# Performance work log

Measured on AMD Instinct MI355X. Metric: run time of the kernel, lower is better.

The kernel has to match this reference:

```python
import jax, jax.numpy as jnp
import numpy as np
import math

B, L, CS, CZ = 1, 512, 256, 128
H, CH, PQ, PV = 8, 32, 4, 8
NUM_BLOCKS = 8
CAT = H * CH + H * PV * 3 + H * PV + H * CZ  # 1536


def _ln(x, g, b, eps=1e-5):
    mu = jnp.mean(x, -1, keepdims=True)
    var = jnp.mean((x - mu) ** 2, -1, keepdims=True)
    return (x - mu) * jax.lax.rsqrt(var + eps) * g + b


def _quat_to_rot(bq, cq, dq):
    # BackboneUpdate: quaternion with implicit a=1, normalized (AF2 Alg. 23)
    norm = jnp.sqrt(1.0 + bq * bq + cq * cq + dq * dq)
    a = 1.0 / norm
    b = bq / norm
    c = cq / norm
    d = dq / norm
    return jnp.stack([
        jnp.stack([a * a + b * b - c * c - d * d, 2 * (b * c - a * d), 2 * (b * d + a * c)], -1),
        jnp.stack([2 * (b * c + a * d), a * a - b * b + c * c - d * d, 2 * (c * d - a * b)], -1),
        jnp.stack([2 * (b * d - a * c), 2 * (c * d + a * b), a * a - b * b - c * c + d * d], -1),
    ], -2)


def _forward(s, z, mask, ln_s_g, ln_s_b, ln_z_g, ln_z_b, w_init, b_init,
             ln_ipa_g, ln_ipa_b, ln_tr_g, ln_tr_b,
             wq, bq, wk, bk, wv, bv, wqp, bqp, wkp, bkp, wvp, bvp,
             wpb, head_w, wo, bo, wt1, bt1, wt2, bt2, wt3, bt3, wbb, bbb):
    s0 = _ln(s, ln_s_g, ln_s_b)
    zn = _ln(z, ln_z_g, ln_z_b)
    sc = s0 @ w_init + b_init
    R = jnp.broadcast_to(jnp.eye(3, dtype=s.dtype), (B, L, 3, 3))
    t = jnp.zeros((B, L, 3), s.dtype)
    wL = math.sqrt(1.0 / 3.0)
    wC = math.sqrt(2.0 / (9.0 * PQ))
    gamma = jax.nn.softplus(head_w)  # [H]
    pair_bias = jnp.einsum('bijc,ch->bhij', zn, wpb)
    mask_bias = (mask[:, None, None, :] - 1.0) * 1e9
    for i in range(NUM_BLOCKS):
        # ---- Invariant Point Attention (AF2 Alg. 22, shared weights) ----
        q = (sc @ wq + bq).reshape(B, L, H, CH)
        k = (sc @ wk + bk).reshape(B, L, H, CH)
        v = (sc @ wv + bv).reshape(B, L, H, CH)
        qp = (sc @ wqp + bqp).reshape(B, L, H, PQ, 3)
        kp = (sc @ wkp + bkp).reshape(B, L, H, PQ, 3)
        vp = (sc @ wvp + bvp).reshape(B, L, H, PV, 3)
        tb = t[:, :, None, None, :]
        qpg = jnp.einsum('blij,blhpj->blhpi', R, qp) + tb  # local -> global
        kpg = jnp.einsum('blij,blhpj->blhpi', R, kp) + tb
        vpg = jnp.einsum('blij,blhpj->blhpi', R, vp) + tb
        scal = jnp.einsum('bihc,bjhc->bhij', q, k) / math.sqrt(CH)
        # sum_p ||qpg_i - kpg_j||^2 via |q|^2 + |k|^2 - 2 q.k (avoids [B,L,L,H,P,3])
        qk = jnp.einsum('bihpx,bjhpx->bhij', qpg, kpg)
        qn = jnp.moveaxis(jnp.sum(qpg ** 2, axis=(-2, -1)), -1, 1)  # [B,H,L]
        kn = jnp.moveaxis(jnp.sum(kpg ** 2, axis=(-2, -1)), -1, 1)
        d2 = qn[..., :, None] + kn[..., None, :] - 2.0 * qk  # [B,H,L,L]
        logits = wL * (scal + pair_bias - 0.5 * wC * gamma[None, :, None, None] * d2) + mask_bias
        a = jax.nn.softmax(logits, axis=-1)
        o = jnp.einsum('bhij,bjhc->bihc', a, v).reshape(B, L, H * CH)
        optg = jnp.einsum('bhij,bjhpx->bihpx', a, vpg)
        optl = jnp.einsum('blji,blhpj->blhpi', R, optg - tb)  # R^T (o - t)
        onrm = jnp.sqrt(jnp.sum(optl ** 2, -1) + 1e-8)  # [B,L,H,PV]
        opair = jnp.einsum('bhij,bijc->bihc', a, zn).reshape(B, L, H * CZ)
        cat = jnp.concatenate([o, optl.reshape(B, L, H * PV * 3), onrm.reshape(B, L, H * PV), opair], -1)
        ipa_up = cat @ wo + bo
        sc = _ln(sc + ipa_up, ln_ipa_g, ln_ipa_b)  # dropout = identity (eval)
        # ---- transition ----
        tr = jax.nn.relu(sc @ wt1 + bt1)
        tr = jax.nn.relu(tr @ wt2 + bt2)
        tr = (tr @ wt3 + bt3) * mask[..., None]
        sc = _ln(sc + tr, ln_tr_g, ln_tr_b)
        # ---- backbone update + frame composition ----
        upd = sc @ wbb + bbb  # [B,L,6]
        dR = _quat_to_rot(upd[..., 0], upd[..., 1], upd[..., 2])
        dt = upd[..., 3:6] * mask[..., None]
        t = jnp.einsum('blij,blj->bli', R, dt) + t
        R = jnp.einsum('blij,bljk->blik', R, dR)
        if i < NUM_BLOCKS - 1:
            R = jax.lax.stop_gradient(R)  # stop_rotation_gradients
    return sc, R, t


def setup_inputs() -> dict:
    key = jax.random.key(0)
    ks = jax.random.split(key, 20)
    w = lambda k, shape, sc=0.05: jax.random.normal(k, shape, jnp.float32) * sc
    inp = dict(
        s=jax.random.normal(ks[0], (B, L, CS), jnp.float32),
        z=jax.random.normal(ks[1], (B, L, L, CZ), jnp.float32),
        mask=jnp.ones((B, L), jnp.float32),
        ln_s_g=jnp.ones((CS,), jnp.float32), ln_s_b=jnp.zeros((CS,), jnp.float32),
        ln_z_g=jnp.ones((CZ,), jnp.float32), ln_z_b=jnp.zeros((CZ,), jnp.float32),
        w_init=w(ks[2], (CS, CS)), b_init=jnp.zeros((CS,), jnp.float32),
        ln_ipa_g=jnp.ones((CS,), jnp.float32), ln_ipa_b=jnp.zeros((CS,), jnp.float32),
        ln_tr_g=jnp.ones((CS,), jnp.float32), ln_tr_b=jnp.zeros((CS,), jnp.float32),
        wq=w(ks[3], (CS, H * CH)), bq=jnp.zeros((H * CH,), jnp.float32),
        wk=w(ks[4], (CS, H * CH)), bk=jnp.zeros((H * CH,), jnp.float32),
        wv=w(ks[5], (CS, H * CH)), bv=jnp.zeros((H * CH,), jnp.float32),
        wqp=w(ks[6], (CS, H * PQ * 3)), bqp=jnp.zeros((H * PQ * 3,), jnp.float32),
        wkp=w(ks[7], (CS, H * PQ * 3)), bkp=jnp.zeros((H * PQ * 3,), jnp.float32),
        wvp=w(ks[8], (CS, H * PV * 3)), bvp=jnp.zeros((H * PV * 3,), jnp.float32),
        wpb=w(ks[9], (CZ, H)),
        head_w=jnp.zeros((H,), jnp.float32),
        wo=w(ks[10], (CAT, CS), 0.02), bo=jnp.zeros((CS,), jnp.float32),
        wt1=w(ks[11], (CS, CS)), bt1=jnp.zeros((CS,), jnp.float32),
        wt2=w(ks[12], (CS, CS)), bt2=jnp.zeros((CS,), jnp.float32),
        wt3=w(ks[13], (CS, CS)), bt3=jnp.zeros((CS,), jnp.float32),
        wbb=w(ks[14], (CS, 6)), bbb=jnp.zeros((6,), jnp.float32),
    )
    return inp


def reference(s, z, mask, ln_s_g, ln_s_b, ln_z_g, ln_z_b, w_init, b_init,
              ln_ipa_g, ln_ipa_b, ln_tr_g, ln_tr_b,
              wq, bq, wk, bk, wv, bv, wqp, bqp, wkp, bkp, wvp, bvp,
              wpb, head_w, wo, bo, wt1, bt1, wt2, bt2, wt3, bt3, wbb, bbb):
    return _forward(s, z, mask, ln_s_g, ln_s_b, ln_z_g, ln_z_b, w_init, b_init,
                    ln_ipa_g, ln_ipa_b, ln_tr_g, ln_tr_b,
                    wq, bq, wk, bk, wv, bv, wqp, bqp, wkp, bkp, wvp, bvp,
                    wpb, head_w, wo, bo, wt1, bt1, wt2, bt2, wt3, bt3, wbb, bbb)
```

## Files before the change

### kernel.cpp

```cpp
#include <hip/hip_runtime.h>
#include <hip/hip_bf16.h>
#include <hip/hip_fp16.h>
#include <math.h>

#define Lq 512
#define CSd 256
#define CZd 128
#define Hd 8
#define CHd 32
#define PQd 4
#define PVd 8
#define CATd 1536
#define NPROJ 1152

typedef __attribute__((ext_vector_type(4))) float floatx4;
typedef __attribute__((ext_vector_type(8))) short shortx8;

#define OFF_SC      0
#define OFF_PB      393216
#define OFF_P       1441792
#define OFF_QN      2031616
#define OFF_KN      2035712
#define OFF_A16     2039808
#define OFF_CAT     4136960
#define OFF_S0      4923392
#define OFF_R       5054464
#define OFF_T       5059072
#define OFF_GAMMA   5060608
#define OFF_MASKB   5060616
#define OFF_BCAT    5061128
#define OFF_WINITP  5062280
#define OFF_WT1P    5127816
#define OFF_WT2P    5193352
#define OFF_WT3P    5258888
#define OFF_WOP     5324424
#define OFF_WCATP   5717640
#define OFF_QP      6012552
#define OFF_KP      6274696
#define OFF_VP      6536840
#define OFF_SCA16   6798984
#define OFF_ZNT     6930056

#define CAT_LO 786432

#define WLC 0.57735026918962576f
#define WCC 0.23570226039551584f
#define ISC 0.17677669529663687f

__device__ __forceinline__ float wave_sum(float v){
  #pragma unroll
  for (int m=32; m; m>>=1) v += __shfl_xor(v, m);
  return v;
}
__device__ __forceinline__ short f2bf(float v){
  __hip_bfloat16 h = (__hip_bfloat16)v;
  return __builtin_bit_cast(short, h);
}
__device__ __forceinline__ float bf2f(short s){
  unsigned u = ((unsigned)(unsigned short)s) << 16;
  return __builtin_bit_cast(float, u);
}
__device__ __forceinline__ __hip_bfloat16 s2b(short s){
  return __builtin_bit_cast(__hip_bfloat16, s);
}
__device__ __forceinline__ void cat_store(short* __restrict__ catA16, int k, int row, float v){
  size_t off = (((size_t)(k>>5)*512 + row)*4 + ((k>>3)&3))*8 + (k&7);
  short hh = f2bf(v);
  catA16[off]          = hh;
  catA16[off + CAT_LO] = f2bf(v - bf2f(hh));
}

__global__ __launch_bounds__(256) void k_setup(
    const float* __restrict__ bq, const float* __restrict__ bk, const float* __restrict__ bv,
    const float* __restrict__ bqp, const float* __restrict__ bkp, const float* __restrict__ bvp,
    const float* __restrict__ head_w, const float* __restrict__ mask,
    float* __restrict__ bcat, float* __restrict__ gamma,
    float* __restrict__ maskb, float* __restrict__ R, float* __restrict__ t){
  int k = blockIdx.x*256 + threadIdx.x;
  if (k < NPROJ){
    float v;
    if      (k < 256) v = bq[k];
    else if (k < 512) v = bk[k-256];
    else if (k < 768) v = bv[k-512];
    else if (k < 864) v = bqp[k-768];
    else if (k < 960) v = bkp[k-864];
    else              v = bvp[k-960];
    bcat[k] = v;
    return;
  }
  k -= NPROJ;
  if (k < Hd){ gamma[k] = log1pf(expf(head_w[k])); return; }
  k -= Hd;
  if (k < Lq){ maskb[k] = (mask[k] - 1.f)*1e9f; return; }
  k -= Lq;
  if (k < Lq){
    #pragma unroll
    for (int ii=0; ii<9; ii++) R[k*9+ii] = (ii==0||ii==4||ii==8) ? 1.f : 0.f;
    t[k*3] = 0.f; t[k*3+1] = 0.f; t[k*3+2] = 0.f;
  }
}

__global__ __launch_bounds__(256) void k_pack(
    const float* __restrict__ W, int K, int N, __hip_bfloat16* __restrict__ out){
  int idx = blockIdx.x*256 + threadIdx.x;
  if (idx >= K*N) return;
  int j = idx & 7, lane = (idx>>3) & 63, rest = idx >> 9;
  int nt = N >> 4;
  int tn = rest % nt, tk = rest / nt;
  int k = tk*32 + (lane>>4)*8 + j;
  int n = tn*16 + (lane&15);
  float v = W[(size_t)k*N + n];
  short h = f2bf(v);
  short l = f2bf(v - bf2f(h));
  size_t base = (size_t)rest*1024 + (idx & 511);
  out[base]       = s2b(h);
  out[base + 512] = s2b(l);
}

__global__ __launch_bounds__(256) void k_pack_cat(
    const float* __restrict__ wq, const float* __restrict__ wk, const float* __restrict__ wv,
    const float* __restrict__ wqp, const float* __restrict__ wkp, const float* __restrict__ wvp,
    __hip_bfloat16* __restrict__ out){
  int idx = blockIdx.x*256 + threadIdx.x;
  if (idx >= CSd*NPROJ) return;
  int j = idx & 7, lane = (idx>>3) & 63, rest = idx >> 9;
  const int nt = NPROJ >> 4;
  int tn = rest % nt, tk = rest / nt;
  int k = tk*32 + (lane>>4)*8 + j;
  int n = tn*16 + (lane&15);
  float v;
  if      (n < 256) v = wq[k*256 + n];
  else if (n < 512) v = wk[k*256 + n-256];
  else if (n < 768) v = wv[k*256 + n-512];
  else if (n < 864) v = wqp[k*96 + n-768];
  else if (n < 960) v = wkp[k*96 + n-864];
  else              v = wvp[k*192 + n-960];
  short h = f2bf(v);
  short l = f2bf(v - bf2f(h));
  size_t base = (size_t)rest*1024 + (idx & 511);
  out[base]       = s2b(h);
  out[base + 512] = s2b(l);
}

template<int NST>
__global__ __launch_bounds__(256) void k_gemm_mfma(
    const float* __restrict__ A, int K,
    const __hip_bfloat16* __restrict__ Bp, int N,
    const float* __restrict__ bias,
    float* __restrict__ Cf,
    int relu, const float* __restrict__ rowscale){
  int tid = threadIdx.x;
  int wave = tid>>6, lane = tid&63;
  int i0 = blockIdx.y*64 + wave*16;
  int n0 = blockIdx.x*(NST*16);
  int quad = lane>>4, l16 = lane&15;
  floatx4 acc[NST] = {};
  const int ntiles = N >> 4;
  const float* arow = A + (size_t)(i0 + l16)*K + quad*8;
  const __hip_bfloat16* bbase = Bp + ((size_t)(n0>>4))*1024 + (size_t)(lane&63)*8;
  for (int k0=0; k0<K; k0+=32){
    float4 v0 = *(const float4*)(arow + k0);
    float4 v1 = *(const float4*)(arow + k0 + 4);
    float av[8] = {v0.x,v0.y,v0.z,v0.w,v1.x,v1.y,v1.z,v1.w};
    shortx8 ahi, alo;
    #pragma unroll
    for (int j=0; j<8; j++){
      short h = f2bf(av[j]);
      ahi[j] = h;
      alo[j] = f2bf(av[j] - bf2f(h));
    }
    const __hip_bfloat16* bt = bbase + (size_t)(k0>>5)*ntiles*1024;
    #pragma unroll
    for (int s=0; s<NST; s++){
      shortx8 bhi = *(const shortx8*)(bt + s*1024);
      shortx8 blo = *(const shortx8*)(bt + s*1024 + 512);
      acc[s] = __builtin_amdgcn_mfma_f32_16x16x32_bf16(ahi, bhi, acc[s], 0, 0, 0);
      acc[s] = __builtin_amdgcn_mfma_f32_16x16x32_bf16(alo, bhi, acc[s], 0, 0, 0);
      acc[s] = __builtin_amdgcn_mfma_f32_16x16x32_bf16(ahi, blo, acc[s], 0, 0, 0);
    }
  }
  #pragma unroll
  for (int s=0; s<NST; s++){
    int n = n0 + s*16 + l16;
    float bs = bias ? bias[n] : 0.f;
    #pragma unroll
    for (int r=0; r<4; r++){
      int m = i0 + quad*4 + r;
      float v = acc[s][r] + bs;
      if (relu) v = fmaxf(v, 0.f);
      if (rowscale) v *= rowscale[m];
      Cf[(size_t)m*N + n] = v;
    }
  }
}

__global__ __launch_bounds__(256) void k_cvtA(
    const float* __restrict__ sc, short* __restrict__ scA16){
  int idx = blockIdx.x*256 + threadIdx.x;
  int i = idx>>5, c5 = idx&31;
  int c0 = c5*8, kc = c5>>2, quad = c5&3;
  float4 v0 = *(const float4*)(sc + (size_t)i*CSd + c0);
  float4 v1 = *(const float4*)(sc + (size_t)i*CSd + c0 + 4);
  float av[8] = {v0.x,v0.y,v0.z,v0.w,v1.x,v1.y,v1.z,v1.w};
  shortx8 hi, lo;
  #pragma unroll
  for (int j=0; j<8; j++){
    short h = f2bf(av[j]);
    hi[j] = h; lo[j] = f2bf(av[j] - bf2f(h));
  }
  size_t off = ((size_t)(kc*512 + i)*4 + quad)*8;
  *(shortx8*)(scA16 + off)          = hi;
  *(shortx8*)(scA16 + off + 131072) = lo;
}

__global__ __launch_bounds__(256) void k_gemm_proj(
    const short* __restrict__ scA16,
    const __hip_bfloat16* __restrict__ Bp,
    const float* __restrict__ bias,
    float* __restrict__ Cf){
  int tid = threadIdx.x;
  int wave = tid>>6, lane = tid&63;
  int i0 = blockIdx.y*64 + wave*16;
  int n0 = blockIdx.x*32;
  int quad = lane>>4, l16 = lane&15;
  floatx4 acc[2] = {};
  const short* abase = scA16 + ((size_t)(i0 + l16)*4 + quad)*8;
  const __hip_bfloat16* bbase = Bp + ((size_t)(n0>>4))*1024 + (size_t)lane*8;
  #pragma unroll
  for (int kc=0; kc<8; kc++){
    shortx8 ahi = *(const shortx8*)(abase + kc*16384);
    shortx8 alo = *(const shortx8*)(abase + kc*16384 + 131072);
    const __hip_bfloat16* bt = bbase + (size_t)kc*72*1024;
    #pragma unroll
    for (int s=0; s<2; s++){
      shortx8 bhi = *(const shortx8*)(bt + s*1024);
      shortx8 blo = *(const shortx8*)(bt + s*1024 + 512);
      acc[s] = __builtin_amdgcn_mfma_f32_16x16x32_bf16(ahi, bhi, acc[s], 0, 0, 0);
      acc[s] = __builtin_amdgcn_mfma_f32_16x16x32_bf16(alo, bhi, acc[s], 0, 0, 0);
      acc[s] = __builtin_amdgcn_mfma_f32_16x16x32_bf16(ahi, blo, acc[s], 0, 0, 0);
    }
  }
  #pragma unroll
  for (int s=0; s<2; s++){
    int n = n0 + s*16 + l16;
    float bs = bias[n];
    #pragma unroll
    for (int r=0; r<4; r++)
      Cf[(size_t)(i0 + quad*4 + r)*NPROJ + n] = acc[s][r] + bs;
  }
}

__global__ __launch_bounds__(256) void k_gemm_ipa(
    const short* __restrict__ catA16, const __hip_bfloat16* __restrict__ Bp,
    const float* __restrict__ bias, float* __restrict__ C0, float* __restrict__ C1){
  int tid = threadIdx.x;
  int wave = tid>>6, lane = tid&63;
  int ks = blockIdx.y >> 3;
  int i0 = (blockIdx.y & 7)*64 + wave*16;
  int n0 = blockIdx.x*16;
  int quad = lane>>4, l16 = lane&15;
  floatx4 acc = {};
  const short* abase = catA16 + (size_t)(ks*24)*16384 + (size_t)(i0 + l16)*32 + quad*8;
  const __hip_bfloat16* bbase = Bp + ((size_t)(ks*24*16 + (n0>>4)))*1024 + (size_t)lane*8;
  #pragma unroll
  for (int kc=0; kc<24; kc++){
    shortx8 ahi = *(const shortx8*)(abase + kc*16384);
    shortx8 alo = *(const shortx8*)(abase + kc*16384 + CAT_LO);
    const __hip_bfloat16* bt = bbase + (size_t)kc*16*1024;
    shortx8 bhi = *(const shortx8*)bt;
    shortx8 blo = *(const shortx8*)(bt + 512);
    acc = __builtin_amdgcn_mfma_f32_16x16x32_bf16(ahi, bhi, acc, 0, 0, 0);
    acc = __builtin_amdgcn_mfma_f32_16x16x32_bf16(alo, bhi, acc, 0, 0, 0);
    acc = __builtin_amdgcn_mfma_f32_16x16x32_bf16(ahi, blo, acc, 0, 0, 0);
  }
  float* C = ks ? C1 : C0;
  int n = n0 + l16;
  float bs = ks ? 0.f : bias[n];
  #pragma unroll
  for (int r=0; r<4; r++)
    C[(size_t)(i0 + quad*4 + r)*CSd + n] = acc[r] + bs;
}

__global__ __launch_bounds__(256) void k_addln(
    const float* __restrict__ x, const float* __restrict__ y,
    const float* __restrict__ g, const float* __restrict__ b,
    float* __restrict__ out){
  __shared__ float red[4];
  int row = blockIdx.x, tid = threadIdx.x;
  float v = x[row*CSd + tid];
  if (y) v += y[row*CSd + tid];
  int wid = tid>>6, lane = tid&63;
  float s = wave_sum(v);
  if (lane==0) red[wid] = s;
  __syncthreads();
  float mu = (red[0]+red[1]+red[2]+red[3]) * (1.f/CSd);
  __syncthreads();
  float d = v - mu;
  float s2 = wave_sum(d*d);
  if (lane==0) red[wid] = s2;
  __syncthreads();
  float var = (red[0]+red[1]+red[2]+red[3]) * (1.f/CSd);
  float rs = rsqrtf(var + 1e-5f);
  out[row*CSd + tid] = d*rs*g[tid] + b[tid];
}

__global__ __launch_bounds__(1024, 4) void k_lnz_pb(
    const float* __restrict__ z, const float* __restrict__ g, const float* __restrict__ b,
    const float* __restrict__ wpb, __half* __restrict__ pb, __hip_bfloat16* __restrict__ znt){
  __shared__ float Zt[64*129];
  __shared__ float wpbht[8*129];
  __shared__ float gl[128], bl[128];
  int tid = threadIdx.x;
  size_t row0 = (size_t)blockIdx.x*64;
  int ib = (int)(row0 >> 9), j0 = (int)(row0 & 511);
  {
    int c = tid>>3, h = tid&7;
    wpbht[h*129 + c] = wpb[tid];
  }
  if (tid < 128){ gl[tid] = g[tid]; bl[tid] = b[tid]; }
  {
    int w = tid>>6, lane = tid&63;
    #pragma unroll
    for (int it=0; it<4; it++){
      int row = it*16 + w;
      const float2 v = *(const float2*)(z + (row0+row)*(size_t)CZd + lane*2);
      Zt[row*129 + lane*2]     = v.x;
      Zt[row*129 + lane*2 + 1] = v.y;
    }
  }
  __syncthreads();
  {
    int r = tid>>4, q = tid&15;
    int rot = 2*(q>>2);
    float S1=0.f, S2=0.f;
    float zv[8];
    #pragma unroll
    for (int i=0; i<8; i++){
      int ii = (i + rot) & 7;
      float v = Zt[r*129 + q*8 + ii];
      zv[i] = v;
      S1 += v; S2 += v*v;
    }
    S1 += __shfl_xor(S1,1); S2 += __shfl_xor(S2,1);
    S1 += __shfl_xor(S1,2); S2 += __shfl_xor(S2,2);
    S1 += __shfl_xor(S1,4); S2 += __shfl_xor(S2,4);
    S1 += __shfl_xor(S1,8); S2 += __shfl_xor(S2,8);
    float mu = S1 * (1.f/128.f);
    float var = S2 * (1.f/128.f) - mu*mu;
    float rs = rsqrtf(var + 1e-5f);
    float d[8] = {};
    #pragma unroll
    for (int i=0; i<8; i++){
      int ii = (i + rot) & 7;
      int c = q*8 + ii;
      float znv = (zv[i]-mu)*rs*gl[c] + bl[c];
      Zt[r*129 + c] = znv;
      #pragma unroll
      for (int h=0; h<8; h++) d[h] += znv * wpbht[h*129 + c];
    }
    #pragma unroll
    for (int h=0; h<8; h++){
      d[h] += __shfl_xor(d[h],1);
      d[h] += __shfl_xor(d[h],2);
      d[h] += __shfl_xor(d[h],4);
      d[h] += __shfl_xor(d[h],8);
    }
    if (q == 0){
      #pragma unroll
      for (int h=0; h<8; h++)
        pb[((size_t)(h*Lq + ib))*Lq + j0 + r] = __float2half(d[h]);
    }
  }
  __syncthreads();
  {
    int c = tid>>3, jg = tid&7;
    int jb = jg*8;
    unsigned int o[4];
    #pragma unroll
    for (int k=0; k<4; k++){
      float z0 = Zt[(jb+2*k)*129 + c];
      float z1 = Zt[(jb+2*k+1)*129 + c];
      o[k] = ((unsigned int)(unsigned short)f2bf(z0)) |
             (((unsigned int)(unsigned short)f2bf(z1)) << 16);
    }
    unsigned short* zo = (unsigned short*)znt;
    uint4 pk = make_uint4(o[0],o[1],o[2],o[3]);
    *(uint4*)(zo + ((size_t)(ib*128 + c))*512 + j0 + jb) = pk;
  }
}

__global__ __launch_bounds__(256) void k_packqkv(
    const float* __restrict__ P, const float* __restrict__ R, const float* __restrict__ t,
    const float* __restrict__ gamma, int zfill,
    float* __restrict__ Qp, __hip_bfloat16* __restrict__ Kp, __hip_bfloat16* __restrict__ Vp,
    float* __restrict__ qn, float* __restrict__ kn){
  int idx = blockIdx.x*256 + threadIdx.x;
  int region = idx >> 15;
  int rem = idx & 32767;
  if (region == 0){
    int oct = rem & 7, h = (rem>>3)&7, j = rem>>6;
    float v[8] = {0.f,0.f,0.f,0.f,0.f,0.f,0.f,0.f};
    const float* Prow = P + (size_t)j*NPROJ;
    if (oct < 4){
      float4 a = *(const float4*)(Prow + 256 + h*CHd + oct*8);
      float4 b4 = *(const float4*)(Prow + 256 + h*CHd + oct*8 + 4);
      v[0]=a.x; v[1]=a.y; v[2]=a.z; v[3]=a.w; v[4]=b4.x; v[5]=b4.y; v[6]=b4.z; v[7]=b4.w;
    } else if (oct < 6){
      const float* kp = Prow + 864 + h*12;
      float4 k0 = *(const float4*)kp;
      float4 k1 = *(const float4*)(kp+4);
      float4 k2 = *(const float4*)(kp+8);
      float kv[12] = {k0.x,k0.y,k0.z,k0.w,k1.x,k1.y,k1.z,k1.w,k2.x,k2.y,k2.z,k2.w};
      float Rl[9];
      #pragma unroll
      for (int ii=0; ii<9; ii++) Rl[ii] = R[j*9+ii];
      float tv[3] = {t[j*3], t[j*3+1], t[j*3+2]};
      float gvals[12];
      #pragma unroll
      for (int p=0; p<4; p++)
        #pragma unroll
        for (int ax=0; ax<3; ax++)
          gvals[p*3+ax] = Rl[ax*3]*kv[p*3] + Rl[ax*3+1]*kv[p*3+1] + Rl[ax*3+2]*kv[p*3+2] + tv[ax];
      if (oct == 4){
        #pragma unroll
        for (int m=0; m<8; m++) v[m] = gvals[m];
      } else {
        #pragma unroll
        for (int m=0; m<4; m++) v[m] = gvals[8+m];
        float acc = 0.f;
        #pragma unroll
        for (int m=0; m<12; m++) acc += gvals[m]*gvals[m];
        kn[j*Hd + h] = acc;
      }
    } else {
      if (!zfill) return;
    }
    shortx8 hi, lo;
    #pragma unroll
    for (int m=0; m<8; m++){
      short hh = f2bf(v[m]);
      hi[m] = hh; lo[m] = f2bf(v[m] - bf2f(hh));
    }
    int kc = oct>>2, jt = j>>4, l16 = j&15, quad = oct&3;
    size_t base = (size_t)((h*2+kc)*32 + jt)*1024 + (quad*16+l16)*8;
    short* kp16 = (short*)Kp;
    *(shortx8*)(kp16 + base)       = hi;
    *(shortx8*)(kp16 + base + 512) = lo;
  } else if (region == 1){
    int n = rem & 63, h = (rem>>6)&7, jg = rem>>9;
    int jb = jg*8;
    float v[8] = {0.f,0.f,0.f,0.f,0.f,0.f,0.f,0.f};
    if (n < 32){
      #pragma unroll
      for (int m=0; m<8; m++) v[m] = P[(size_t)(jb+m)*NPROJ + 512 + h*CHd + n];
    } else if (n < 56){
      int p = (n-32)/3, ax = (n-32)%3;
      #pragma unroll
      for (int m=0; m<8; m++){
        int j = jb+m;
        const float* vp = P + (size_t)j*NPROJ + 960 + h*24 + p*3;
        const float* Rr = R + j*9 + ax*3;
        v[m] = Rr[0]*vp[0] + Rr[1]*vp[1] + Rr[2]*vp[2] + t[j*3+ax];
      }
    } else {
      if (!zfill) return;
    }
    shortx8 hi, lo;
    #pragma unroll
    for (int m=0; m<8; m++){
      short hh = f2bf(v[m]);
      hi[m] = hh; lo[m] = f2bf(v[m] - bf2f(hh));
    }
    int kc2 = jg>>2, w = n>>4, l16 = n&15, quad = jg&3;
    size_t base = (size_t)((h*16+kc2)*4 + w)*1024 + (quad*16+l16)*8;
    short* vp16 = (short*)Vp;
    *(shortx8*)(vp16 + base)       = hi;
    *(shortx8*)(vp16 + base + 512) = lo;
  } else {
    int oct = rem & 7, h = (rem>>3)&7, i = rem>>6;
    float v[8] = {0.f,0.f,0.f,0.f,0.f,0.f,0.f,0.f};
    const float* Prow = P + (size_t)i*NPROJ;
    if (oct < 4){
      float4 a = *(const float4*)(Prow + h*CHd + oct*8);
      float4 b4 = *(const float4*)(Prow + h*CHd + oct*8 + 4);
      const float sc = WLC*ISC;
      v[0]=a.x*sc; v[1]=a.y*sc; v[2]=a.z*sc; v[3]=a.w*sc;
      v[4]=b4.x*sc; v[5]=b4.y*sc; v[6]=b4.z*sc; v[7]=b4.w*sc;
    } else if (oct < 6){
      const float* qp = Prow + 768 + h*12;
      float4 k0 = *(const float4*)qp;
      float4 k1 = *(const float4*)(qp+4);
      float4 k2 = *(const float4*)(qp+8);
      float kv[12] = {k0.x,k0.y,k0.z,k0.w,k1.x,k1.y,k1.z,k1.w,k2.x,k2.y,k2.z,k2.w};
      float Rl[9];
      #pragma unroll
      for (int ii=0; ii<9; ii++) Rl[ii] = R[i*9+ii];
      float tv[3] = {t[i*3], t[i*3+1], t[i*3+2]};
      float gvals[12];
      #pragma unroll
      for (int p=0; p<4; p++)
        #pragma unroll
        for (int ax=0; ax<3; ax++)
          gvals[p*3+ax] = Rl[ax*3]*kv[p*3] + Rl[ax*3+1]*kv[p*3+1] + Rl[ax*3+2]*kv[p*3+2] + tv[ax];
      float sc = WLC*WCC*gamma[h];
      if (oct == 4){
        #pragma unroll
        for (int m=0; m<8; m++) v[m] = gvals[m]*sc;
      } else {
        #pragma unroll
        for (int m=0; m<4; m++) v[m] = gvals[8+m]*sc;
        float acc = 0.f;
        #pragma unroll
        for (int m=0; m<12; m++) acc += gvals[m]*gvals[m];
        qn[i*Hd + h] = acc;
      }
    } else {
      if (!zfill) return;
    }
    float* qrow = Qp + ((size_t)h*512 + i)*64 + oct*8;
    *(float4*)qrow       = make_float4(v[0],v[1],v[2],v[3]);
    *(float4*)(qrow + 4) = make_float4(v[4],v[5],v[6],v[7]);
  }
}

__global__ __launch_bounds__(1024) void k_attn(
    const float* __restrict__ Qp, const __hip_bfloat16* __restrict__ Kp,
    const __hip_bfloat16* __restrict__ Vp,
    const float* __restrict__ qn, const float* __restrict__ kn,
    const __half* __restrict__ pb, const float* __restrict__ maskb,
    const float* __restrict__ gamma,
    const float* __restrict__ R, const float* __restrict__ t,
    __hip_bfloat16* __restrict__ a16hi,
    short* __restrict__ catA16){
  __shared__ float At[16][516];
  __shared__ short AbfH[16*4*16*8];
  __shared__ short AbfL[16*4*16*8];
  __shared__ float Pv[3][16][68];
  __shared__ float Ot[16][36];
  __shared__ float qnL[16];
  int tid = threadIdx.x;
  int i0 = blockIdx.x*16, h = blockIdx.y;
  int wave = tid>>6, lane = tid&63, quad = lane>>4, l16 = lane&15;
  int kg = wave>>2, ng = wave&3;
  float gam = gamma[h];
  float coef = 0.5f*WLC*WCC*gam;
  if (tid < 16) qnL[tid] = qn[(i0+tid)*Hd + h];
  __syncthreads();
  const float* qrow = Qp + ((size_t)h*512 + i0 + l16)*64 + quad*8;
  shortx8 qhi[2], qlo[2];
  #pragma unroll
  for (int kc=0; kc<2; kc++){
    float4 v0 = *(const float4*)(qrow + kc*32);
    float4 v1 = *(const float4*)(qrow + kc*32 + 4);
    float av[8] = {v0.x,v0.y,v0.z,v0.w,v1.x,v1.y,v1.z,v1.w};
    #pragma unroll
    for (int j=0; j<8; j++){
      short hh = f2bf(av[j]);
      qhi[kc][j] = hh; qlo[kc][j] = f2bf(av[j] - bf2f(hh));
    }
  }
  #pragma unroll
  for (int it=0; it<2; it++){
    int jt = it*16 + wave;
    floatx4 acc = {};
    #pragma unroll
    for (int kc=0; kc<2; kc++){
      const __hip_bfloat16* bt = Kp + (size_t)((h*2+kc)*32 + jt)*1024 + lane*8;
      shortx8 bhi = *(const shortx8*)bt;
      shortx8 blo = *(const shortx8*)(bt + 512);
      acc = __builtin_amdgcn_mfma_f32_16x16x32_bf16(qhi[kc], bhi, acc, 0, 0, 0);
      acc = __builtin_amdgcn_mfma_f32_16x16x32_bf16(qlo[kc], bhi, acc, 0, 0, 0);
      acc = __builtin_amdgcn_mfma_f32_16x16x32_bf16(qhi[kc], blo, acc, 0, 0, 0);
    }
    int j = jt*16 + l16;
    float knj = kn[j*Hd + h];
    float mbj = maskb[j];
    #pragma unroll
    for (int r=0; r<4; r++){
      int i = quad*4 + r;
      float pbv = __half2float(pb[((size_t)(h*Lq) + i0 + i)*Lq + j]);
      At[i][j] = acc[r] + WLC*pbv + mbj - coef*(qnL[i] + knj);
    }
  }
  __syncthreads();
  {
    int w = wave;
    float v[8];
    float m = -1e30f;
    #pragma unroll
    for (int k=0; k<8; k++){ v[k] = At[w][lane + 64*k]; m = fmaxf(m, v[k]); }
    #pragma unroll
    for (int msk=32; msk; msk>>=1) m = fmaxf(m, __shfl_xor(m, msk));
    float ssum = 0.f;
    #pragma unroll
    for (int k=0; k<8; k++){ float e = __expf(v[k]-m); v[k]=e; ssum += e; }
    #pragma unroll
    for (int msk=32; msk; msk>>=1) ssum += __shfl_xor(ssum, msk);
    float inv = 1.f/ssum;
    #pragma unroll
    for (int k=0; k<8; k++){
      int cc = lane + 64*k;
      float p = v[k]*inv;
      short hh = f2bf(p);
      short ll = f2bf(p - bf2f(hh));
      a16hi[(((size_t)(i0+w)*16 + (cc>>5))*8 + h)*32 + (cc&31)] = s2b(hh);
      int off = ((((cc>>5)*4 + ((cc>>3)&3))*16 + w)<<3) + (cc&7);
      AbfH[off] = hh;
      AbfL[off] = ll;
    }
  }
  __syncthreads();
  floatx4 acc2 = {};
  #pragma unroll
  for (int kk=0; kk<4; kk++){
    int kc2 = kg*4 + kk;
    int aoff = (((kc2*4 + quad)*16 + l16))<<3;
    shortx8 ahi = *(const shortx8*)&AbfH[aoff];
    shortx8 alo = *(const shortx8*)&AbfL[aoff];
    const __hip_bfloat16* bt = Vp + (size_t)((h*16+kc2)*4 + ng)*1024 + lane*8;
    shortx8 bhi = *(const shortx8*)bt;
    shortx8 blo = *(const shortx8*)(bt + 512);
    acc2 = __builtin_amdgcn_mfma_f32_16x16x32_bf16(ahi, bhi, acc2, 0, 0, 0);
    acc2 = __builtin_amdgcn_mfma_f32_16x16x32_bf16(alo, bhi, acc2, 0, 0, 0);
    acc2 = __builtin_amdgcn_mfma_f32_16x16x32_bf16(ahi, blo, acc2, 0, 0, 0);
  }
  if (kg > 0){
    #pragma unroll
    for (int r=0;r<4;r++) Pv[kg-1][quad*4+r][ng*16+l16] = acc2[r];
  }
  __syncthreads();
  if (kg == 0){
    int n = ng*16 + l16;
    #pragma unroll
    for (int r=0;r<4;r++){
      int i = quad*4+r;
      float v = acc2[r] + Pv[0][i][n] + Pv[1][i][n] + Pv[2][i][n];
      if (n < 32) cat_store(catA16, h*CHd + n, i0+i, v);
      else        Ot[i][n-32] = v;
    }
  }
  __syncthreads();
  if (tid < 128){
    int i = tid>>3, p = tid&7, gi = i0+i;
    float o0 = Ot[i][p*3], o1 = Ot[i][p*3+1], o2 = Ot[i][p*3+2];
    float d0 = o0 - t[gi*3], d1 = o1 - t[gi*3+1], d2 = o2 - t[gi*3+2];
    const float* Rm = R + gi*9;
    float l0 = Rm[0]*d0 + Rm[3]*d1 + Rm[6]*d2;
    float l1 = Rm[1]*d0 + Rm[4]*d1 + Rm[7]*d2;
    float l2 = Rm[2]*d0 + Rm[5]*d1 + Rm[8]*d2;
    int kb = 256 + h*24 + p*3;
    cat_store(catA16, kb,   gi, l0);
    cat_store(catA16, kb+1, gi, l1);
    cat_store(catA16, kb+2, gi, l2);
    cat_store(catA16, 448 + h*8 + p, gi, sqrtf(l0*l0 + l1*l1 + l2*l2 + 1e-8f));
  }
}

__global__ __launch_bounds__(512) void k_opair_mfma(
    const __hip_bfloat16* __restrict__ a16hi,
    const __hip_bfloat16* __restrict__ znt, short* __restrict__ catA16){
  int i = blockIdx.x;
  int tid = threadIdx.x;
  int wave = tid>>6, lane = tid&63, quad = lane>>4, l16 = lane&15;
  int nt = wave;
  floatx4 acc = {};
  const __hip_bfloat16* abase_h = a16hi + ((size_t)i*16*8 + (l16&7))*32 + quad*8;
  const __hip_bfloat16* zb = znt + ((size_t)i*128 + nt*16 + l16)*512 + quad*8;
  #pragma unroll
  for (int kt=0; kt<16; kt++){
    shortx8 ah = *(const shortx8*)(abase_h + kt*256);
    shortx8 b0 = *(const shortx8*)(zb + kt*32);
    acc = __builtin_amdgcn_mfma_f32_16x16x32_bf16(ah, b0, acc, 0, 0, 0);
  }
  if (quad < 2){
    #pragma unroll
    for (int r=0; r<4; r++){
      int h = quad*4 + r;
      cat_store(catA16, 512 + h*CZd + nt*16 + l16, i, acc[r]);
    }
  }
}

__device__ __forceinline__ void gemm_bf16w(
    const short* __restrict__ AHp, const short* __restrict__ ALp,
    short* __restrict__ OH, short* __restrict__ OL, float (*Yf)[260],
    const __hip_bfloat16* __restrict__ Wp, const float* __restrict__ bias,
    bool relu, int tid){
  int wave = tid>>6, lane = tid&63, quad = lane>>4, l16 = lane&15;
  floatx4 acc = {};
  #pragma unroll
  for (int kc=0; kc<8; kc++){
    int aoff = (((kc*4 + quad)*16 + l16))<<3;
    shortx8 ahi = *(const shortx8*)&AHp[aoff];
    shortx8 alo = *(const shortx8*)&ALp[aoff];
    const __hip_bfloat16* bt = Wp + (size_t)(kc*16 + wave)*1024 + lane*8;
    shortx8 bhi = *(const shortx8*)bt;
    shortx8 blo = *(const shortx8*)(bt + 512);
    acc = __builtin_amdgcn_mfma_f32_16x16x32_bf16(ahi, bhi, acc, 0, 0, 0);
    acc = __builtin_amdgcn_mfma_f32_16x16x32_bf16(alo, bhi, acc, 0, 0, 0);
    acc = __builtin_amdgcn_mfma_f32_16x16x32_bf16(ahi, blo, acc, 0, 0, 0);
  }
  int n = wave*16 + l16;
  float bs = bias[n];
  #pragma unroll
  for (int r=0;r<4;r++){
    float v = acc[r] + bs;
    if (relu) v = fmaxf(v, 0.f);
    int row = quad*4 + r;
    if (OH){
      short hh = f2bf(v);
      int off = ((((n>>5)*4 + ((n>>3)&3))*16 + row)<<3) + (n&7);
      OH[off] = hh;
      OL[off] = f2bf(v - bf2f(hh));
    } else {
      Yf[row][n] = v;
    }
  }
}

__global__ __launch_bounds__(1024) void k_mega(
    float* __restrict__ scb, const float* __restrict__ ipa, const float* __restrict__ ipa2,
    const float* __restrict__ gi_, const float* __restrict__ bi_,
    const __hip_bfloat16* __restrict__ W1, const float* __restrict__ c1,
    const __hip_bfloat16* __restrict__ W2, const float* __restrict__ c2,
    const __hip_bfloat16* __restrict__ W3, const float* __restrict__ c3,
    const float* __restrict__ gt_, const float* __restrict__ bt_,
    const float* __restrict__ mask,
    const float* __restrict__ wbb, const float* __restrict__ bbb,
    float* __restrict__ R, float* __restrict__ t, short* __restrict__ scA16){
  __shared__ float As[16][260], Bs[16][260];
  __shared__ short AH[2][4096], AL[2][4096];
  __shared__ float rA[16][33], rB[16][33];
  __shared__ float mv[16][2];
  __shared__ float u6p[16][6][2];
  int tid = threadIdx.x;
  int i0 = blockIdx.x*16;
  int r = (tid>>5)&15, c5 = tid&31, c0 = c5*8;
  float v[8];
  if (tid < 512){
    const float* sr = scb + (size_t)(i0+r)*CSd + c0;
    const float* ir = ipa + (size_t)(i0+r)*CSd + c0;
    const float* ir2 = ipa2 + (size_t)(i0+r)*CSd + c0;
    float s1=0.f, s2=0.f;
    #pragma unroll
    for (int k2=0;k2<8;k2++){ float x = sr[k2] + ir[k2] + ir2[k2]; v[k2]=x; s1+=x; s2+=x*x; }
    rA[r][c5]=s1; rB[r][c5]=s2;
  }
  __syncthreads();
  if (tid<16){
    float s1=0.f,s2=0.f;
    #pragma unroll
    for (int c=0;c<32;c++){ s1+=rA[tid][c]; s2+=rB[tid][c]; }
    float mu = s1*(1.f/CSd), var = s2*(1.f/CSd) - mu*mu;
    mv[tid][0]=mu; mv[tid][1]=rsqrtf(var+1e-5f);
  }
  __syncthreads();
  if (tid < 512){
    float mu=mv[r][0], rs=mv[r][1];
    #pragma unroll
    for (int k2=0;k2<8;k2++){
      int col = c0+k2;
      float o = (v[k2]-mu)*rs*gi_[col] + bi_[col];
      As[r][col] = o;
      short hh = f2bf(o);
      int off = ((((col>>5)*4 + ((col>>3)&3))*16 + r)<<3) + (col&7);
      AH[0][off] = hh;
      AL[0][off] = f2bf(o - bf2f(hh));
    }
  }
  __syncthreads();
  gemm_bf16w(AH[0], AL[0], AH[1], AL[1], nullptr, W1, c1, true, tid);
  __syncthreads();
  gemm_bf16w(AH[1], AL[1], AH[0], AL[0], nullptr, W2, c2, true, tid);
  __syncthreads();
  gemm_bf16w(AH[0], AL[0], nullptr, nullptr, Bs, W3, c3, false, tid);
  __syncthreads();
  if (tid < 512){
    float mk = mask[i0+r];
    float s1=0.f, s2=0.f;
    #pragma unroll
    for (int k2=0;k2<8;k2++){ float x = As[r][c0+k2] + Bs[r][c0+k2]*mk; v[k2]=x; s1+=x; s2+=x*x; }
    rA[r][c5]=s1; rB[r][c5]=s2;
  }
  __syncthreads();
  if (tid<16){
    float s1=0.f,s2=0.f;
    #pragma unroll
    for (int c=0;c<32;c++){ s1+=rA[tid][c]; s2+=rB[tid][c]; }
    float mu = s1*(1.f/CSd), var = s2*(1.f/CSd) - mu*mu;
    mv[tid][0]=mu; mv[tid][1]=rsqrtf(var+1e-5f);
  }
  __syncthreads();
  if (tid < 512){
    float mu=mv[r][0], rs=mv[r][1];
    float* out = scb + (size_t)(i0+r)*CSd + c0;
    shortx8 hi, lo;
    #pragma unroll
    for (int k2=0;k2<8;k2++){
      int col = c0+k2;
      float o = (v[k2]-mu)*rs*gt_[col] + bt_[col];
      As[r][col] = o;
      out[k2] = o;
      short hh = f2bf(o);
      hi[k2] = hh; lo[k2] = f2bf(o - bf2f(hh));
    }
    size_t off = ((size_t)((c5>>2)*512 + i0 + r)*4 + (c5&3))*8;
    *(shortx8*)(scA16 + off)          = hi;
    *(shortx8*)(scA16 + off + 131072) = lo;
  }
  __syncthreads();
  if (tid < 192){
    int rr = tid/12, o = (tid%12)>>1, half = tid&1;
    float acc = half ? 0.f : bbb[o];
    int kb = half*128;
    for (int k2=kb; k2<kb+128; k2++) acc += As[rr][k2]*wbb[k2*6+o];
    u6p[rr][o][half] = acc;
  }
  __syncthreads();
  if (tid < 16){
    int gidx = i0 + tid;
    float uu[6];
    #pragma unroll
    for (int o=0;o<6;o++) uu[o] = u6p[tid][o][0] + u6p[tid][o][1];
    float bq = uu[0], cq = uu[1], dq = uu[2];
    float norm = sqrtf(1.f + bq*bq + cq*cq + dq*dq);
    float a = 1.f/norm, b_ = bq/norm, c_ = cq/norm, d_ = dq/norm;
    float dR[9];
    dR[0] = a*a + b_*b_ - c_*c_ - d_*d_; dR[1] = 2.f*(b_*c_ - a*d_); dR[2] = 2.f*(b_*d_ + a*c_);
    dR[3] = 2.f*(b_*c_ + a*d_); dR[4] = a*a - b_*b_ + c_*c_ - d_*d_; dR[5] = 2.f*(c_*d_ - a*b_);
    dR[6] = 2.f*(b_*d_ - a*c_); dR[7] = 2.f*(c_*d_ + a*b_); dR[8] = a*a - b_*b_ - c_*c_ + d_*d_;
    float mk = mask[gidx];
    float dt0 = uu[3]*mk, dt1 = uu[4]*mk, dt2 = uu[5]*mk;
    float Rm[9];
    #pragma unroll
    for (int ii=0; ii<9; ii++) Rm[ii] = R[gidx*9+ii];
    t[gidx*3]   += Rm[0]*dt0 + Rm[1]*dt1 + Rm[2]*dt2;
    t[gidx*3+1] += Rm[3]*dt0 + Rm[4]*dt1 + Rm[5]*dt2;
    t[gidx*3+2] += Rm[6]*dt0 + Rm[7]*dt1 + Rm[8]*dt2;
    #pragma unroll
    for (int ii=0; ii<3; ii++)
      #pragma unroll
      for (int jj=0; jj<3; jj++)
        R[gidx*9 + ii*3 + jj] = Rm[ii*3]*dR[jj] + Rm[ii*3+1]*dR[3+jj] + Rm[ii*3+2]*dR[6+jj];
  }
}

__global__ __launch_bounds__(256) void k_writeout(
    const float* __restrict__ sc, const float* __restrict__ R, const float* __restrict__ t,
    float* __restrict__ out){
  int idx = blockIdx.x*256 + threadIdx.x;
  if      (idx < 131072) out[idx] = sc[idx];
  else if (idx < 135680) out[idx] = R[idx-131072];
  else if (idx < 137216) out[idx] = t[idx-135680];
}

extern "C" void kernel_launch(void* const* d_in, const int* in_sizes, int n_in,
                              void* d_out, int out_size, void* d_ws, size_t ws_size,
                              hipStream_t stream){
  const float* s      = (const float*)d_in[0];
  const float* z      = (const float*)d_in[1];
  const float* mask   = (const float*)d_in[2];
  const float* ln_s_g = (const float*)d_in[3];
  const float* ln_s_b = (const float*)d_in[4];
  const float* ln_z_g = (const float*)d_in[5];
  const float* ln_z_b = (const float*)d_in[6];
  const float* w_init = (const float*)d_in[7];
  const float* b_init = (const float*)d_in[8];
  const float* ln_ipa_g = (const float*)d_in[9];
  const float* ln_ipa_b = (const float*)d_in[10];
  const float* ln_tr_g  = (const float*)d_in[11];
  const float* ln_tr_b  = (const float*)d_in[12];
  const float* wq = (const float*)d_in[13]; const float* bq = (const float*)d_in[14];
  const float* wk = (const float*)d_in[15]; const float* bk = (const float*)d_in[16];
  const float* wv = (const float*)d_in[17]; const float* bv = (const float*)d_in[18];
  const float* wqp = (const float*)d_in[19]; const float* bqp = (const float*)d_in[20];
  const float* wkp = (const float*)d_in[21]; const float* bkp = (const float*)d_in[22];
  const float* wvp = (const float*)d_in[23]; const float* bvp = (const float*)d_in[24];
  const float* wpb = (const float*)d_in[25];
  const float* head_w = (const float*)d_in[26];
  const float* wo = (const float*)d_in[27]; const float* bo = (const float*)d_in[28];
  const float* wt1 = (const float*)d_in[29]; const float* bt1 = (const float*)d_in[30];
  const float* wt2 = (const float*)d_in[31]; const float* bt2 = (const float*)d_in[32];
  const float* wt3 = (const float*)d_in[33]; const float* bt3 = (const float*)d_in[34];
  const float* wbb = (const float*)d_in[35]; const float* bbb = (const float*)d_in[36];

  float* W = (float*)d_ws;
  float* scb   = W + OFF_SC;
  __half*  pbb  = (__half*)(W + OFF_PB);
  float* Pb    = W + OFF_P;
  float* ipa2b = W + OFF_P + 262144;
  float* qnb   = W + OFF_QN;
  float* knb   = W + OFF_KN;
  __hip_bfloat16* a16hi = (__hip_bfloat16*)(W + OFF_A16);
  short* catA16 = (short*)(W + OFF_CAT);
  float* s0b   = W + OFF_S0;
  float* Rb    = W + OFF_R;
  float* tb    = W + OFF_T;
  float* gammab= W + OFF_GAMMA;
  float* maskb = W + OFF_MASKB;
  float* bcat  = W + OFF_BCAT;
  __hip_bfloat16* WinitP = (__hip_bfloat16*)(W + OFF_WINITP);
  __hip_bfloat16* Wt1P   = (__hip_bfloat16*)(W + OFF_WT1P);
  __hip_bfloat16* Wt2P   = (__hip_bfloat16*)(W + OFF_WT2P);
  __hip_bfloat16* Wt3P   = (__hip_bfloat16*)(W + OFF_WT3P);
  __hip_bfloat16* WoP    = (__hip_bfloat16*)(W + OFF_WOP);
  __hip_bfloat16* WcatP  = (__hip_bfloat16*)(W + OFF_WCATP);
  float* Qp = W + OFF_QP;
  __hip_bfloat16* Kp = (__hip_bfloat16*)(W + OFF_KP);
  __hip_bfloat16* Vp = (__hip_bfloat16*)(W + OFF_VP);
  short* scA16 = (short*)(W + OFF_SCA16);
  __hip_bfloat16* znt = (__hip_bfloat16*)(W + OFF_ZNT);

  k_setup<<<9, 256, 0, stream>>>(bq,bk,bv,bqp,bkp,bvp, head_w, mask, bcat, gammab, maskb, Rb, tb);
  k_pack_cat<<<CSd*NPROJ/256, 256, 0, stream>>>(wq,wk,wv,wqp,wkp,wvp, WcatP);
  k_pack<<<256,  256, 0, stream>>>(w_init, CSd, CSd, WinitP);
  k_pack<<<1536, 256, 0, stream>>>(wo, CATd, CSd, WoP);
  k_pack<<<256,  256, 0, stream>>>(wt1, CSd, CSd, Wt1P);
  k_pack<<<256,  256, 0, stream>>>(wt2, CSd, CSd, Wt2P);
  k_pack<<<256,  256, 0, stream>>>(wt3, CSd, CSd, Wt3P);

  k_addln<<<Lq, 256, 0, stream>>>(s, nullptr, ln_s_g, ln_s_b, s0b);
  k_gemm_mfma<4><<<dim3(4,8), 256, 0, stream>>>(s0b, CSd, WinitP, CSd, b_init, scb, 0, nullptr);
  k_cvtA<<<64, 256, 0, stream>>>(scb, scA16);
  k_lnz_pb<<<Lq*Lq/64, 1024, 0, stream>>>(z, ln_z_g, ln_z_b, wpb, pbb, znt);

  for (int it=0; it<8; ++it){
    k_gemm_proj<<<dim3(36,8), 256, 0, stream>>>(scA16, WcatP, bcat, Pb);
    k_packqkv<<<384, 256, 0, stream>>>(Pb, Rb, tb, gammab, (it==0)?1:0,
                                       Qp, Kp, Vp, qnb, knb);
    k_attn<<<dim3(32,8), 1024, 0, stream>>>(Qp, Kp, Vp, qnb, knb, pbb, maskb, gammab, Rb, tb,
                                            a16hi, catA16);
    k_opair_mfma<<<Lq, 512, 0, stream>>>(a16hi, znt, catA16);
    k_gemm_ipa<<<dim3(16,16), 256, 0, stream>>>(catA16, WoP, bo, Pb, ipa2b);
    k_mega<<<32, 1024, 0, stream>>>(scb, Pb, ipa2b, ln_ipa_g, ln_ipa_b,
                                    Wt1P, bt1, Wt2P, bt2, Wt3P, bt3,
                                    ln_tr_g, ln_tr_b, mask, wbb, bbb, Rb, tb, scA16);
  }
  k_writeout<<<536, 256, 0, stream>>>(scb, Rb, tb, (float*)d_out);
}
```

Measured before the change: 848.5 us.

## Increase grid parallelism in projection and output GEMMs; simplify pair-bias weights

Halves the N tile of the per-block projection GEMM so it launches twice as many workgroups. Splits the output GEMM's K dimension four ways instead of two, writing four partial results that the fused transition kernel now sums. The z layernorm/pair-bias kernel drops its shared-memory staging of gamma, beta and wpb and reads them straight from global memory with vector loads. The aim is better GPU occupancy for small GEMMs, at the cost of more partial-sum traffic and redundant A-operand loads.

Result: slower. 918.0 us (+8.2%).

```diff
diff --git a/kernel.cpp b/kernel.cpp
--- a/kernel.cpp
+++ b/kernel.cpp
@@ -221,38 +221,32 @@
   int tid = threadIdx.x;
   int wave = tid>>6, lane = tid&63;
   int i0 = blockIdx.y*64 + wave*16;
-  int n0 = blockIdx.x*32;
+  int n0 = blockIdx.x*16;
   int quad = lane>>4, l16 = lane&15;
-  floatx4 acc[2] = {};
+  floatx4 acc = {};
   const short* abase = scA16 + ((size_t)(i0 + l16)*4 + quad)*8;
-  const __hip_bfloat16* bbase = Bp + ((size_t)(n0>>4))*1024 + (size_t)lane*8;
+  const __hip_bfloat16* bbase = Bp + (size_t)blockIdx.x*1024 + (size_t)lane*8;
   #pragma unroll
   for (int kc=0; kc<8; kc++){
     shortx8 ahi = *(const shortx8*)(abase + kc*16384);
     shortx8 alo = *(const shortx8*)(abase + kc*16384 + 131072);
     const __hip_bfloat16* bt = bbase + (size_t)kc*72*1024;
-    #pragma unroll
-    for (int s=0; s<2; s++){
-      shortx8 bhi = *(const shortx8*)(bt + s*1024);
-      shortx8 blo = *(const shortx8*)(bt + s*1024 + 512);
-      acc[s] = __builtin_amdgcn_mfma_f32_16x16x32_bf16(ahi, bhi, acc[s], 0, 0, 0);
-      acc[s] = __builtin_amdgcn_mfma_f32_16x16x32_bf16(alo, bhi, acc[s], 0, 0, 0);
-      acc[s] = __builtin_amdgcn_mfma_f32_16x16x32_bf16(ahi, blo, acc[s], 0, 0, 0);
-    }
-  }
-  #pragma unroll
-  for (int s=0; s<2; s++){
-    int n = n0 + s*16 + l16;
-    float bs = bias[n];
-    #pragma unroll
-    for (int r=0; r<4; r++)
-      Cf[(size_t)(i0 + quad*4 + r)*NPROJ + n] = acc[s][r] + bs;
-  }
+    shortx8 bhi = *(const shortx8*)bt;
+    shortx8 blo = *(const shortx8*)(bt + 512);
+    acc = __builtin_amdgcn_mfma_f32_16x16x32_bf16(ahi, bhi, acc, 0, 0, 0);
+    acc = __builtin_amdgcn_mfma_f32_16x16x32_bf16(alo, bhi, acc, 0, 0, 0);
+    acc = __builtin_amdgcn_mfma_f32_16x16x32_bf16(ahi, blo, acc, 0, 0, 0);
+  }
+  int n = n0 + l16;
+  float bs = bias[n];
+  #pragma unroll
+  for (int r=0; r<4; r++)
+    Cf[(size_t)(i0 + quad*4 + r)*NPROJ + n] = acc[r] + bs;
 }
 
 __global__ __launch_bounds__(256) void k_gemm_ipa(
     const short* __restrict__ catA16, const __hip_bfloat16* __restrict__ Bp,
-    const float* __restrict__ bias, float* __restrict__ C0, float* __restrict__ C1){
+    const float* __restrict__ bias, float* __restrict__ C){
   int tid = threadIdx.x;
   int wave = tid>>6, lane = tid&63;
   int ks = blockIdx.y >> 3;
@@ -260,10 +254,10 @@
   int n0 = blockIdx.x*16;
   int quad = lane>>4, l16 = lane&15;
   floatx4 acc = {};
-  const short* abase = catA16 + (size_t)(ks*24)*16384 + (size_t)(i0 + l16)*32 + quad*8;
-  const __hip_bfloat16* bbase = Bp + ((size_t)(ks*24*16 + (n0>>4)))*1024 + (size_t)lane*8;
-  #pragma unroll
-  for (int kc=0; kc<24; kc++){
+  const short* abase = catA16 + (size_t)(ks*12)*16384 + (size_t)(i0 + l16)*32 + quad*8;
+  const __hip_bfloat16* bbase = Bp + ((size_t)(ks*12*16 + blockIdx.x))*1024 + (size_t)lane*8;
+  #pragma unroll
+  for (int kc=0; kc<12; kc++){
     shortx8 ahi = *(const shortx8*)(abase + kc*16384);
     shortx8 alo = *(const shortx8*)(abase + kc*16384 + CAT_LO);
     const __hip_bfloat16* bt = bbase + (size_t)kc*16*1024;
@@ -273,12 +267,12 @@
     acc = __builtin_amdgcn_mfma_f32_16x16x32_bf16(alo, bhi, acc, 0, 0, 0);
     acc = __builtin_amdgcn_mfma_f32_16x16x32_bf16(ahi, blo, acc, 0, 0, 0);
   }
-  float* C = ks ? C1 : C0;
+  float* Cp = C + (size_t)ks*131072;
   int n = n0 + l16;
   float bs = ks ? 0.f : bias[n];
   #pragma unroll
   for (int r=0; r<4; r++)
-    C[(size_t)(i0 + quad*4 + r)*CSd + n] = acc[r] + bs;
+    Cp[(size_t)(i0 + quad*4 + r)*CSd + n] = acc[r] + bs;
 }
 
 __global__ __launch_bounds__(256) void k_addln(
@@ -308,16 +302,9 @@
     const float* __restrict__ z, const float* __restrict__ g, const float* __restrict__ b,
     const float* __restrict__ wpb, __half* __restrict__ pb, __hip_bfloat16* __restrict__ znt){
   __shared__ float Zt[64*129];
-  __shared__ float wpbht[8*129];
-  __shared__ float gl[128], bl[128];
   int tid = threadIdx.x;
   size_t row0 = (size_t)blockIdx.x*64;
   int ib = (int)(row0 >> 9), j0 = (int)(row0 & 511);
-  {
-    int c = tid>>3, h = tid&7;
-    wpbht[h*129 + c] = wpb[tid];
-  }
-  if (tid < 128){ gl[tid] = g[tid]; bl[tid] = b[tid]; }
   {
     int w = tid>>6, lane = tid&63;
     #pragma unroll
@@ -353,10 +340,12 @@
     for (int i=0; i<8; i++){
       int ii = (i + rot) & 7;
       int c = q*8 + ii;
-      float znv = (zv[i]-mu)*rs*gl[c] + bl[c];
+      float znv = (zv[i]-mu)*rs*g[c] + b[c];
       Zt[r*129 + c] = znv;
-      #pragma unroll
-      for (int h=0; h<8; h++) d[h] += znv * wpbht[h*129 + c];
+      const float4 w0 = *(const float4*)(wpb + c*8);
+      const float4 w1 = *(const float4*)(wpb + c*8 + 4);
+      d[0] += znv*w0.x; d[1] += znv*w0.y; d[2] += znv*w0.z; d[3] += znv*w0.w;
+      d[4] += znv*w1.x; d[5] += znv*w1.y; d[6] += znv*w1.z; d[7] += znv*w1.w;
     }
     #pragma unroll
     for (int h=0; h<8; h++){
@@ -719,7 +708,7 @@
 }
 
 __global__ __launch_bounds__(1024) void k_mega(
-    float* __restrict__ scb, const float* __restrict__ ipa, const float* __restrict__ ipa2,
+    float* __restrict__ scb, const float* __restrict__ ipa,
     const float* __restrict__ gi_, const float* __restrict__ bi_,
     const __hip_bfloat16* __restrict__ W1, const float* __restrict__ c1,
     const __hip_bfloat16* __restrict__ W2, const float* __restrict__ c2,
@@ -739,11 +728,16 @@
   float v[8];
   if (tid < 512){
     const float* sr = scb + (size_t)(i0+r)*CSd + c0;
-    const float* ir = ipa + (size_t)(i0+r)*CSd + c0;
-    const float* ir2 = ipa2 + (size_t)(i0+r)*CSd + c0;
+    const float* p0 = ipa + (size_t)(i0+r)*CSd + c0;
+    const float* p1 = p0 + 131072;
+    const float* p2 = p0 + 262144;
+    const float* p3 = p0 + 393216;
     float s1=0.f, s2=0.f;
     #pragma unroll
-    for (int k2=0;k2<8;k2++){ float x = sr[k2] + ir[k2] + ir2[k2]; v[k2]=x; s1+=x; s2+=x*x; }
+    for (int k2=0;k2<8;k2++){
+      float x = sr[k2] + p0[k2] + p1[k2] + p2[k2] + p3[k2];
+      v[k2]=x; s1+=x; s2+=x*x;
+    }
     rA[r][c5]=s1; rB[r][c5]=s2;
   }
   __syncthreads();
@@ -888,7 +882,6 @@
   float* scb   = W + OFF_SC;
   __half*  pbb  = (__half*)(W + OFF_PB);
   float* Pb    = W + OFF_P;
-  float* ipa2b = W + OFF_P + 262144;
   float* qnb   = W + OFF_QN;
   float* knb   = W + OFF_KN;
   __hip_bfloat16* a16hi = (__hip_bfloat16*)(W + OFF_A16);
@@ -925,14 +918,14 @@
   k_lnz_pb<<<Lq*Lq/64, 1024, 0, stream>>>(z, ln_z_g, ln_z_b, wpb, pbb, znt);
 
   for (int it=0; it<8; ++it){
-    k_gemm_proj<<<dim3(36,8), 256, 0, stream>>>(scA16, WcatP, bcat, Pb);
+    k_gemm_proj<<<dim3(72,8), 256, 0, stream>>>(scA16, WcatP, bcat, Pb);
     k_packqkv<<<384, 256, 0, stream>>>(Pb, Rb, tb, gammab, (it==0)?1:0,
                                        Qp, Kp, Vp, qnb, knb);
     k_attn<<<dim3(32,8), 1024, 0, stream>>>(Qp, Kp, Vp, qnb, knb, pbb, maskb, gammab, Rb, tb,
                                             a16hi, catA16);
     k_opair_mfma<<<Lq, 512, 0, stream>>>(a16hi, znt, catA16);
-    k_gemm_ipa<<<dim3(16,16), 256, 0, stream>>>(catA16, WoP, bo, Pb, ipa2b);
-    k_mega<<<32, 1024, 0, stream>>>(scb, Pb, ipa2b, ln_ipa_g, ln_ipa_b,
+    k_gemm_ipa<<<dim3(16,32), 256, 0, stream>>>(catA16, WoP, bo, Pb);
+    k_mega<<<32, 1024, 0, stream>>>(scb, Pb, ln_ipa_g, ln_ipa_b,
                                     Wt1P, bt1, Wt2P, bt2, Wt3P, bt3,
                                     ln_tr_g, ln_tr_b, mask, wbb, bbb, Rb, tb, scA16);
   }
```
